# Optimization experiments

Measured on AMD Instinct MI355X. Metric: run time of the kernel, lower is better.

## Reference

```python
import jax, jax.numpy as jnp
import numpy as np

N_HEAD = 16
NEG = -1e9

def setup_inputs() -> dict:
    key = jax.random.key(0)
    ks = jax.random.split(key, 11)
    B, T, D = 2, 2048, 1024
    s = 0.02
    return {
        "x": jax.random.normal(ks[0], (B, T, D), jnp.float32),
        "mask": jax.random.randint(ks[1], (B, T), 0, 2).astype(bool),
        "wq": jax.random.normal(ks[2], (D, D), jnp.float32) * s,
        "bq": jax.random.normal(ks[3], (D,), jnp.float32) * s,
        "wk": jax.random.normal(ks[4], (D, D), jnp.float32) * s,
        "bk": jax.random.normal(ks[5], (D,), jnp.float32) * s,
        "wv": jax.random.normal(ks[6], (D, D), jnp.float32) * s,
        "bv": jax.random.normal(ks[7], (D,), jnp.float32) * s,
        "wp": jax.random.normal(ks[8], (D, D), jnp.float32) * s,
        "bp": jax.random.normal(ks[9], (D,), jnp.float32) * s,
    }

def reference(x, mask, wq, bq, wk, bk, wv, bv, wp, bp):
    B, T, V = x.shape
    H = N_HEAD
    hd = V // H
    # project and split heads: [B, H, T, hd]
    def heads(w, b):
        return (x @ w + b).reshape(B, T, H, hd).transpose(0, 2, 1, 3)
    q = heads(wq, bq)
    k = heads(wk, bk)
    v = heads(wv, bv)
    # scores [B, H, T, T]
    att = jnp.einsum("bhqd,bhkd->bhqk", q, k) * (1.0 / jnp.sqrt(jnp.float32(hd)))
    # key-padding mask: True -> masked. broadcast [B,1,1,T] == torch's [B,1,T,T]
    att = jnp.where(mask[:, None, None, :], NEG, att)
    att = jax.nn.softmax(att, axis=-1)
    out = jnp.einsum("bhqk,bhkd->bhqd", att, v)  # [B,H,T,hd]
    out = out.transpose(0, 2, 1, 3).reshape(B, T, V)
    out = out @ wp + bp
    # dropout is identity in eval mode
    return out, att
```

## Files before the change

### kernel.cpp

```cpp
#include <hip/hip_runtime.h>
#include <stdint.h>
#include <stddef.h>


typedef __attribute__((ext_vector_type(8))) short short8;
typedef __attribute__((ext_vector_type(4))) float f32x4;

#define LDS_AS __attribute__((address_space(3)))
#define GLB_AS __attribute__((address_space(1)))

static __device__ __forceinline__ unsigned short f2bf(float f) {
  union { float f; uint32_t u; } v; v.f = f;
  uint32_t u = v.u;
  return (unsigned short)((u + 0x7fffu + ((u >> 16) & 1u)) >> 16);
}

static __device__ __forceinline__ void gload16(const void* g, void* l) {
  __builtin_amdgcn_global_load_lds((const GLB_AS uint32_t*)g, (LDS_AS uint32_t*)l, 16, 0, 0);
}

static __device__ __forceinline__ f32x4 mfma16(short8 a, short8 b, f32x4 c) {
  return __builtin_amdgcn_mfma_f32_16x16x32_bf16(a, b, c, 0, 0, 0);
}

__global__ void k_convert_x(const float* __restrict__ x, unsigned short* __restrict__ xb) {
  int i = blockIdx.x * 256 + threadIdx.x;
  float4 v = ((const float4*)x)[i];
  ushort4 o;
  o.x = f2bf(v.x); o.y = f2bf(v.y); o.z = f2bf(v.z); o.w = f2bf(v.w);
  ((ushort4*)xb)[i] = o;
}

__global__ void k_mask(const int* __restrict__ m, float* __restrict__ madd) {
  int i = blockIdx.x * 256 + threadIdx.x;
  madd[i] = m[i] ? -1e9f : 0.0f;
}

__global__ void k_transpose_w(const float* __restrict__ w0, const float* __restrict__ w1,
                              const float* __restrict__ w2, const float* __restrict__ w3,
                              unsigned short* __restrict__ o0, unsigned short* __restrict__ o1,
                              unsigned short* __restrict__ o2, unsigned short* __restrict__ o3) {
  int bx = blockIdx.x;
  int which = bx >> 8, tile = bx & 255;
  const float* w = which == 0 ? w0 : which == 1 ? w1 : which == 2 ? w2 : w3;
  unsigned short* o = which == 0 ? o0 : which == 1 ? o1 : which == 2 ? o2 : o3;
  int k0 = (tile >> 4) << 6, n0 = (tile & 15) << 6;
  __shared__ float t[64][65];
  int tid = threadIdx.x;
  int r = tid >> 4, c4 = (tid & 15) << 2;
#pragma unroll
  for (int i = 0; i < 4; i++) {
    int row = r + (i << 4);
    float4 v = *(const float4*)(w + (size_t)(k0 + row) * 1024 + n0 + c4);
    t[row][c4] = v.x; t[row][c4 + 1] = v.y; t[row][c4 + 2] = v.z; t[row][c4 + 3] = v.w;
  }
  __syncthreads();
#pragma unroll
  for (int i = 0; i < 4; i++) {
    int n = r + (i << 4);
    ushort4 ov;
    ov.x = f2bf(t[c4 + 0][n]); ov.y = f2bf(t[c4 + 1][n]);
    ov.z = f2bf(t[c4 + 2][n]); ov.w = f2bf(t[c4 + 3][n]);
    *(ushort4*)(o + (size_t)(n0 + n) * 1024 + k0 + c4) = ov;
  }
}

static __device__ __forceinline__ void gemm_tile(const unsigned short* __restrict__ A,
                                                 const unsigned short* __restrict__ Bt,
                                                 int m0, int n0,
                                                 f32x4 acc[4][4], char* ldsA, char* ldsB) {
  const int tid = threadIdx.x;
  const int l = tid & 63;
  const int wr = tid >> 7;
  const int wc = (tid >> 6) & 1;
  const int arow0 = wr * 64 + (l & 15);
  const int brow0 = wc * 64 + (l & 15);
  const int srow = tid >> 3;
  const int sgi = tid & 7;

  for (int kt = 0; kt < 1024; kt += 64) {
    __syncthreads();
#pragma unroll
    for (int c = 0; c < 4; c++) {
      int row = c * 32 + srow;
      int soff = (sgi ^ (row & 7)) << 3;
      gload16(A + (size_t)(m0 + row) * 1024 + kt + soff, ldsA + (c * 256 + tid) * 16);
      gload16(Bt + (size_t)(n0 + row) * 1024 + kt + soff, ldsB + (c * 256 + tid) * 16);
    }
    asm volatile("s_waitcnt vmcnt(0)" ::: "memory");
    __syncthreads();
#pragma unroll
    for (int ks = 0; ks < 2; ks++) {
      const int kbyte = ks * 64 + ((l >> 4) << 4);
      short8 a[4], b[4];
#pragma unroll
      for (int i = 0; i < 4; i++) {
        int row = arow0 + i * 16;
        a[i] = *(const short8*)(ldsA + row * 128 + (kbyte ^ ((row & 7) << 4)));
      }
#pragma unroll
      for (int j = 0; j < 4; j++) {
        int row = brow0 + j * 16;
        b[j] = *(const short8*)(ldsB + row * 128 + (kbyte ^ ((row & 7) << 4)));
      }
#pragma unroll
      for (int i = 0; i < 4; i++)
#pragma unroll
        for (int j = 0; j < 4; j++)
          acc[i][j] = mfma16(a[i], b[j], acc[i][j]);
    }
  }
}

__global__ __launch_bounds__(256) void k_gemm_qkv(const unsigned short* __restrict__ xb,
    const unsigned short* __restrict__ wqt, const unsigned short* __restrict__ wkt,
    const unsigned short* __restrict__ wvt,
    const float* __restrict__ bq, const float* __restrict__ bk, const float* __restrict__ bv,
    unsigned short* __restrict__ Q, unsigned short* __restrict__ K, unsigned short* __restrict__ Vt) {
  __shared__ __align__(16) char smem[32768];
  char* ldsA = smem;
  char* ldsB = smem + 16384;
  const int mat = blockIdx.y >> 3;
  const int nb = blockIdx.y & 7;
  const unsigned short* Bt = mat == 0 ? wqt : mat == 1 ? wkt : wvt;
  const float* bias = mat == 0 ? bq : mat == 1 ? bk : bv;
  const int m0 = blockIdx.x * 128, n0 = nb * 128;

  f32x4 acc[4][4] = {};
  gemm_tile(xb, Bt, m0, n0, acc, ldsA, ldsB);

  const int tid = threadIdx.x, l = tid & 63;
  const int wr = tid >> 7, wc = (tid >> 6) & 1;
  if (mat < 2) {
    unsigned short* O = (mat == 0) ? Q : K;
#pragma unroll
    for (int j = 0; j < 4; j++) {
      int col = n0 + wc * 64 + j * 16 + (l & 15);
      float bv_ = bias[col];
      int h = col >> 6, d = col & 63;
#pragma unroll
      for (int i = 0; i < 4; i++) {
        int row0 = m0 + wr * 64 + i * 16 + ((l >> 4) << 2);
#pragma unroll
        for (int e = 0; e < 4; e++) {
          int row = row0 + e;
          int b = row >> 11, t = row & 2047;
          O[(((size_t)(b * 16 + h)) * 2048 + t) * 64 + d] = f2bf(acc[i][j][e] + bv_);
        }
      }
    }
  } else {
#pragma unroll
    for (int j = 0; j < 4; j++) {
      int col = n0 + wc * 64 + j * 16 + (l & 15);
      float bv_ = bias[col];
      int h = col >> 6, d = col & 63;
#pragma unroll
      for (int i = 0; i < 4; i++) {
        int row0 = m0 + wr * 64 + i * 16 + ((l >> 4) << 2);
        int b = row0 >> 11, t0 = row0 & 2047;
        ushort4 pk;
        pk.x = f2bf(acc[i][j][0] + bv_);
        pk.y = f2bf(acc[i][j][1] + bv_);
        pk.z = f2bf(acc[i][j][2] + bv_);
        pk.w = f2bf(acc[i][j][3] + bv_);
        *(ushort4*)(Vt + ((size_t)(b * 16 + h) * 64 + d) * 2048 + t0) = pk;
      }
    }
  }
}

__global__ __launch_bounds__(256) void k_gemm_proj(const unsigned short* __restrict__ ctx,
    const unsigned short* __restrict__ wpt, const float* __restrict__ bp,
    float* __restrict__ out) {
  __shared__ __align__(16) char smem[32768];
  char* ldsA = smem;
  char* ldsB = smem + 16384;
  const int m0 = blockIdx.x * 128, n0 = blockIdx.y * 128;
  f32x4 acc[4][4] = {};
  gemm_tile(ctx, wpt, m0, n0, acc, ldsA, ldsB);
  const int tid = threadIdx.x, l = tid & 63;
  const int wr = tid >> 7, wc = (tid >> 6) & 1;
#pragma unroll
  for (int j = 0; j < 4; j++) {
    int col = n0 + wc * 64 + j * 16 + (l & 15);
    float bv_ = bp[col];
#pragma unroll
    for (int i = 0; i < 4; i++) {
      int row0 = m0 + wr * 64 + i * 16 + ((l >> 4) << 2);
#pragma unroll
      for (int e = 0; e < 4; e++)
        out[(size_t)(row0 + e) * 1024 + col] = acc[i][j][e] + bv_;
    }
  }
}

__global__ __launch_bounds__(256) void k_attn(const unsigned short* __restrict__ Q,
    const unsigned short* __restrict__ K, const unsigned short* __restrict__ Vt,
    const float* __restrict__ maskadd, float* __restrict__ att,
    unsigned short* __restrict__ ctx) {
  __shared__ __align__(16) char smem[57344];
  char* Ql = smem;
  char* Kl = smem + 8192;
  char* Vl = smem + 24576;
  char* Pl = smem + 40960;

  const int bid = blockIdx.x;
  const int qb = bid & 31, bh = bid >> 5;
  const int b = bh >> 4, h = bh & 15;
  const int tid = threadIdx.x, w = tid >> 6, l = tid & 63;
  const int qbase = qb * 64;

  const unsigned short* Qg = Q + (size_t)bh * 2048 * 64;
  const unsigned short* Kg = K + (size_t)bh * 2048 * 64;
  const unsigned short* Vg = Vt + (size_t)bh * 64 * 2048;
  const float* mg = maskadd + b * 2048;
  const float scale = 0.125f;

#pragma unroll
  for (int c = 0; c < 2; c++) {
    int g = c * 256 + tid;
    int row = g >> 3, gi = tid & 7;
    gload16(Qg + (size_t)(qbase + row) * 64 + ((gi ^ (row & 7)) << 3), Ql + g * 16);
  }
  asm volatile("s_waitcnt vmcnt(0)" ::: "memory");
  __syncthreads();

  short8 qf[2];
  {
    int row = w * 16 + (l & 15);
#pragma unroll
    for (int ks = 0; ks < 2; ks++) {
      int kbyte = ks * 64 + ((l >> 4) << 4);
      qf[ks] = *(const short8*)(Ql + row * 128 + (kbyte ^ ((row & 7) << 4)));
    }
  }

  float mrow[4], srow[4];
#pragma unroll
  for (int e = 0; e < 4; e++) { mrow[e] = -1e30f; srow[e] = 0.0f; }

  for (int ch = 0; ch < 16; ch++) {
    __syncthreads();
#pragma unroll
    for (int c = 0; c < 4; c++) {
      int g = c * 256 + tid;
      int row = g >> 3, gi = tid & 7;
      gload16(Kg + (size_t)(ch * 128 + row) * 64 + ((gi ^ (row & 7)) << 3), Kl + g * 16);
    }
    asm volatile("s_waitcnt vmcnt(0)" ::: "memory");
    __syncthreads();

    float lv[8][4];
    float cmax[4] = {-1e30f, -1e30f, -1e30f, -1e30f};
#pragma unroll
    for (int nt = 0; nt < 8; nt++) {
      f32x4 s = {};
#pragma unroll
      for (int ks = 0; ks < 2; ks++) {
        int row = nt * 16 + (l & 15);
        int kbyte = ks * 64 + ((l >> 4) << 4);
        short8 kf = *(const short8*)(Kl + row * 128 + (kbyte ^ ((row & 7) << 4)));
        s = mfma16(qf[ks], kf, s);
      }
      int key = ch * 128 + nt * 16 + (l & 15);
      float madd = mg[key];
#pragma unroll
      for (int e = 0; e < 4; e++) {
        lv[nt][e] = s[e] * scale + madd;
        cmax[e] = fmaxf(cmax[e], lv[nt][e]);
      }
    }
#pragma unroll
    for (int e = 0; e < 4; e++) {
      float cs = 0.0f;
#pragma unroll
      for (int nt = 0; nt < 8; nt++) cs += __expf(lv[nt][e] - cmax[e]);
      float mn = fmaxf(mrow[e], cmax[e]);
      srow[e] = srow[e] * __expf(mrow[e] - mn) + cs * __expf(cmax[e] - mn);
      mrow[e] = mn;
    }
  }

  float invs[4];
#pragma unroll
  for (int e = 0; e < 4; e++) {
    float m = mrow[e], s = srow[e];
#pragma unroll
    for (int msk = 1; msk < 16; msk <<= 1) {
      float mo = __shfl_xor(m, msk);
      float so = __shfl_xor(s, msk);
      float mn = fmaxf(m, mo);
      s = s * __expf(m - mn) + so * __expf(mo - mn);
      m = mn;
    }
    mrow[e] = m;
    invs[e] = 1.0f / s;
  }

  f32x4 o[4] = {};
  for (int ch = 0; ch < 16; ch++) {
    __syncthreads();
#pragma unroll
    for (int c = 0; c < 4; c++) {
      int g = c * 256 + tid;
      int row = g >> 3, gi = tid & 7;
      gload16(Kg + (size_t)(ch * 128 + row) * 64 + ((gi ^ (row & 7)) << 3), Kl + g * 16);
    }
#pragma unroll
    for (int c = 0; c < 4; c++) {
      int g = c * 256 + tid;
      int d = g >> 4, gi = tid & 15;
      gload16(Vg + (size_t)d * 2048 + ch * 128 + ((gi ^ (d & 7)) << 3), Vl + g * 16);
    }
    asm volatile("s_waitcnt vmcnt(0)" ::: "memory");
    __syncthreads();

#pragma unroll
    for (int nt = 0; nt < 8; nt++) {
      f32x4 s = {};
#pragma unroll
      for (int ks = 0; ks < 2; ks++) {
        int row = nt * 16 + (l & 15);
        int kbyte = ks * 64 + ((l >> 4) << 4);
        short8 kf = *(const short8*)(Kl + row * 128 + (kbyte ^ ((row & 7) << 4)));
        s = mfma16(qf[ks], kf, s);
      }
      int key = ch * 128 + nt * 16 + (l & 15);
      float madd = mg[key];
#pragma unroll
      for (int e = 0; e < 4; e++) {
        float p = __expf(s[e] * scale + madd - mrow[e]) * invs[e];
        int qrow = qbase + w * 16 + ((l >> 4) << 2) + e;
        att[((size_t)bh * 2048 + qrow) * 2048 + key] = p;
        int pr = w * 16 + ((l >> 4) << 2) + e;
        int cb = (nt * 16 + (l & 15)) * 2;
        *(unsigned short*)(Pl + pr * 256 + (cb ^ ((pr & 7) << 4))) = f2bf(p);
      }
    }
#pragma unroll
    for (int ks = 0; ks < 4; ks++) {
      int prow = w * 16 + (l & 15);
      int kbyte = ks * 64 + ((l >> 4) << 4);
      short8 pa = *(const short8*)(Pl + prow * 256 + (kbyte ^ ((prow & 7) << 4)));
#pragma unroll
      for (int dt = 0; dt < 4; dt++) {
        int vrow = dt * 16 + (l & 15);
        short8 vb = *(const short8*)(Vl + vrow * 256 + (kbyte ^ ((vrow & 7) << 4)));
        o[dt] = mfma16(pa, vb, o[dt]);
      }
    }
  }

#pragma unroll
  for (int dt = 0; dt < 4; dt++) {
#pragma unroll
    for (int e = 0; e < 4; e++) {
      int t = qbase + w * 16 + ((l >> 4) << 2) + e;
      int col = h * 64 + dt * 16 + (l & 15);
      ctx[((size_t)(b * 2048 + t)) * 1024 + col] = f2bf(o[dt][e]);
    }
  }
}

extern "C" void kernel_launch(void* const* d_in, const int* in_sizes, int n_in,
                              void* d_out, int out_size, void* d_ws, size_t ws_size,
                              hipStream_t stream) {
  const float* x  = (const float*)d_in[0];
  const int* mask = (const int*)d_in[1];
  const float* wq = (const float*)d_in[2];
  const float* bq = (const float*)d_in[3];
  const float* wk = (const float*)d_in[4];
  const float* bk = (const float*)d_in[5];
  const float* wv = (const float*)d_in[6];
  const float* bv = (const float*)d_in[7];
  const float* wp = (const float*)d_in[8];
  const float* bp = (const float*)d_in[9];

  float* out = (float*)d_out;
  float* att = out + 4194304;

  char* ws = (char*)d_ws;
  unsigned short* xb  = (unsigned short*)(ws);
  unsigned short* wqt = (unsigned short*)(ws + 8388608);
  unsigned short* wkt = (unsigned short*)(ws + 10485760);
  unsigned short* wvt = (unsigned short*)(ws + 12582912);
  unsigned short* wpt = (unsigned short*)(ws + 14680064);
  unsigned short* Qw  = (unsigned short*)(ws + 16777216);
  unsigned short* Kw  = (unsigned short*)(ws + 25165824);
  unsigned short* Vtw = (unsigned short*)(ws + 33554432);
  unsigned short* ctx = (unsigned short*)(ws + 41943040);
  float* madd         = (float*)(ws + 50331648);

  k_convert_x<<<4096, 256, 0, stream>>>(x, xb);
  k_mask<<<16, 256, 0, stream>>>(mask, madd);
  k_transpose_w<<<1024, 256, 0, stream>>>(wq, wk, wv, wp, wqt, wkt, wvt, wpt);
  k_gemm_qkv<<<dim3(32, 24), 256, 0, stream>>>(xb, wqt, wkt, wvt, bq, bk, bv, Qw, Kw, Vtw);
  k_attn<<<1024, 256, 0, stream>>>(Qw, Kw, Vtw, madd, att, ctx);
  k_gemm_proj<<<dim3(32, 8), 256, 0, stream>>>(ctx, wpt, bp, out);
}
```

Baseline: 276.2 us.

## Stage attention probs in LDS for coalesced stores, double-buffer K, use exp2

Attention probabilities are now written to the fp32 att output from the bf16 P tile in LDS with row-contiguous 16-byte vector stores, instead of scattered per-element stores from the MFMA layout. The P-tile swizzle changes to suit this. The first (statistics) pass double-buffers K tiles across the K and V LDS regions to overlap loads with compute. Scale and mask constants are pre-multiplied by log2(e) so the kernel can use the hardware exp2. Blocks are remapped so consecutive block IDs go to different heads. The risk is that the stored att values are now rounded to bf16 precision, and an extra barrier is added per chunk.

```diff
diff --git a/kernel.cpp b/kernel.cpp
--- a/kernel.cpp
+++ b/kernel.cpp
@@ -13,6 +13,15 @@
   union { float f; uint32_t u; } v; v.f = f;
   uint32_t u = v.u;
   return (unsigned short)((u + 0x7fffu + ((u >> 16) & 1u)) >> 16);
+}
+
+static __device__ __forceinline__ float bf2f(unsigned short h) {
+  union { uint32_t u; float f; } v; v.u = ((uint32_t)h) << 16;
+  return v.f;
+}
+
+static __device__ __forceinline__ float fexp2(float x) {
+  return __builtin_amdgcn_exp2f(x);
 }
 
 static __device__ __forceinline__ void gload16(const void* g, void* l) {
@@ -33,7 +42,7 @@
 
 __global__ void k_mask(const int* __restrict__ m, float* __restrict__ madd) {
   int i = blockIdx.x * 256 + threadIdx.x;
-  madd[i] = m[i] ? -1e9f : 0.0f;
+  madd[i] = m[i] ? -1.44269504e9f : 0.0f;
 }
 
 __global__ void k_transpose_w(const float* __restrict__ w0, const float* __restrict__ w1,
@@ -205,7 +214,7 @@
   char* Vl = smem + 24576;
   char* Pl = smem + 40960;
 
-  const int bid = blockIdx.x;
+  const int bid = (blockIdx.x & 7) * 128 + (blockIdx.x >> 3);
   const int qb = bid & 31, bh = bid >> 5;
   const int b = bh >> 4, h = bh & 15;
   const int tid = threadIdx.x, w = tid >> 6, l = tid & 63;
@@ -215,7 +224,7 @@
   const unsigned short* Kg = K + (size_t)bh * 2048 * 64;
   const unsigned short* Vg = Vt + (size_t)bh * 64 * 2048;
   const float* mg = maskadd + b * 2048;
-  const float scale = 0.125f;
+  const float scale2 = 0.18033688f;
 
 #pragma unroll
   for (int c = 0; c < 2; c++) {
@@ -240,6 +249,81 @@
 #pragma unroll
   for (int e = 0; e < 4; e++) { mrow[e] = -1e30f; srow[e] = 0.0f; }
 
+  {
+#pragma unroll
+    for (int c = 0; c < 4; c++) {
+      int g = c * 256 + tid;
+      int row = g >> 3, gi = tid & 7;
+      gload16(Kg + (size_t)row * 64 + ((gi ^ (row & 7)) << 3), Kl + g * 16);
+    }
+    asm volatile("s_waitcnt vmcnt(0)" ::: "memory");
+    __syncthreads();
+
+    for (int ch = 0; ch < 16; ch++) {
+      char* cur = (ch & 1) ? Vl : Kl;
+      char* nxt = (ch & 1) ? Kl : Vl;
+      if (ch < 15) {
+#pragma unroll
+        for (int c = 0; c < 4; c++) {
+          int g = c * 256 + tid;
+          int row = g >> 3, gi = tid & 7;
+          gload16(Kg + (size_t)((ch + 1) * 128 + row) * 64 + ((gi ^ (row & 7)) << 3),
+                  nxt + g * 16);
+        }
+      }
+
+      float lv[8][4];
+      float cmax[4] = {-1e30f, -1e30f, -1e30f, -1e30f};
+#pragma unroll
+      for (int nt = 0; nt < 8; nt++) {
+        f32x4 s = {};
+#pragma unroll
+        for (int ks = 0; ks < 2; ks++) {
+          int row = nt * 16 + (l & 15);
+          int kbyte = ks * 64 + ((l >> 4) << 4);
+          short8 kf = *(const short8*)(cur + row * 128 + (kbyte ^ ((row & 7) << 4)));
+          s = mfma16(qf[ks], kf, s);
+        }
+        int key = ch * 128 + nt * 16 + (l & 15);
+        float madd = mg[key];
+#pragma unroll
+        for (int e = 0; e < 4; e++) {
+          lv[nt][e] = s[e] * scale2 + madd;
+          cmax[e] = fmaxf(cmax[e], lv[nt][e]);
+        }
+      }
+#pragma unroll
+      for (int e = 0; e < 4; e++) {
+        float cs = 0.0f;
+#pragma unroll
+        for (int nt = 0; nt < 8; nt++) cs += fexp2(lv[nt][e] - cmax[e]);
+        float mn = fmaxf(mrow[e], cmax[e]);
+        srow[e] = srow[e] * fexp2(mrow[e] - mn) + cs * fexp2(cmax[e] - mn);
+        mrow[e] = mn;
+      }
+      asm volatile("s_waitcnt vmcnt(0)" ::: "memory");
+      __syncthreads();
+    }
+  }
+
+  float invs[4];
+#pragma unroll
+  for (int e = 0; e < 4; e++) {
+    float m = mrow[e], s = srow[e];
+#pragma unroll
+    for (int msk = 1; msk < 16; msk <<= 1) {
+      float mo = __shfl_xor(m, msk);
+      float so = __shfl_xor(s, msk);
+      float mn = fmaxf(m, mo);
+      s = s * fexp2(m - mn) + so * fexp2(mo - mn);
+      m = mn;
+    }
+    mrow[e] = m;
+    invs[e] = 1.0f / s;
+  }
+
+  f32x4 o[4] = {};
+  const size_t arowbase = ((size_t)bh * 2048 + qbase) * 2048;
   for (int ch = 0; ch < 16; ch++) {
     __syncthreads();
 #pragma unroll
@@ -248,11 +332,15 @@
       int row = g >> 3, gi = tid & 7;
       gload16(Kg + (size_t)(ch * 128 + row) * 64 + ((gi ^ (row & 7)) << 3), Kl + g * 16);
     }
+#pragma unroll
+    for (int c = 0; c < 4; c++) {
+      int g = c * 256 + tid;
+      int d = g >> 4, gi = tid & 15;
+      gload16(Vg + (size_t)d * 2048 + ch * 128 + ((gi ^ (d & 7)) << 3), Vl + g * 16);
+    }
     asm volatile("s_waitcnt vmcnt(0)" ::: "memory");
     __syncthreads();
 
-    float lv[8][4];
-    float cmax[4] = {-1e30f, -1e30f, -1e30f, -1e30f};
 #pragma unroll
     for (int nt = 0; nt < 8; nt++) {
       f32x4 s = {};
@@ -267,86 +355,39 @@
       float madd = mg[key];
 #pragma unroll
       for (int e = 0; e < 4; e++) {
-        lv[nt][e] = s[e] * scale + madd;
-        cmax[e] = fmaxf(cmax[e], lv[nt][e]);
-      }
-    }
-#pragma unroll
-    for (int e = 0; e < 4; e++) {
-      float cs = 0.0f;
-#pragma unroll
-      for (int nt = 0; nt < 8; nt++) cs += __expf(lv[nt][e] - cmax[e]);
-      float mn = fmaxf(mrow[e], cmax[e]);
-      srow[e] = srow[e] * __expf(mrow[e] - mn) + cs * __expf(cmax[e] - mn);
-      mrow[e] = mn;
-    }
-  }
-
-  float invs[4];
-#pragma unroll
-  for (int e = 0; e < 4; e++) {
-    float m = mrow[e], s = srow[e];
-#pragma unroll
-    for (int msk = 1; msk < 16; msk <<= 1) {
-      float mo = __shfl_xor(m, msk);
-      float so = __shfl_xor(s, msk);
-      float mn = fmaxf(m, mo);
-      s = s * __expf(m - mn) + so * __expf(mo - mn);
-      m = mn;
-    }
-    mrow[e] = m;
-    invs[e] = 1.0f / s;
-  }
-
-  f32x4 o[4] = {};
-  for (int ch = 0; ch < 16; ch++) {
-    __syncthreads();
-#pragma unroll
-    for (int c = 0; c < 4; c++) {
-      int g = c * 256 + tid;
-      int row = g >> 3, gi = tid & 7;
-      gload16(Kg + (size_t)(ch * 128 + row) * 64 + ((gi ^ (row & 7)) << 3), Kl + g * 16);
-    }
-#pragma unroll
-    for (int c = 0; c < 4; c++) {
-      int g = c * 256 + tid;
-      int d = g >> 4, gi = tid & 15;
-      gload16(Vg + (size_t)d * 2048 + ch * 128 + ((gi ^ (d & 7)) << 3), Vl + g * 16);
-    }
-    asm volatile("s_waitcnt vmcnt(0)" ::: "memory");
-    __syncthreads();
-
-#pragma unroll
-    for (int nt = 0; nt < 8; nt++) {
-      f32x4 s = {};
-#pragma unroll
-      for (int ks = 0; ks < 2; ks++) {
-        int row = nt * 16 + (l & 15);
-        int kbyte = ks * 64 + ((l >> 4) << 4);
-        short8 kf = *(const short8*)(Kl + row * 128 + (kbyte ^ ((row & 7) << 4)));
-        s = mfma16(qf[ks], kf, s);
-      }
-      int key = ch * 128 + nt * 16 + (l & 15);
-      float madd = mg[key];
-#pragma unroll
-      for (int e = 0; e < 4; e++) {
-        float p = __expf(s[e] * scale + madd - mrow[e]) * invs[e];
-        int qrow = qbase + w * 16 + ((l >> 4) << 2) + e;
-        att[((size_t)bh * 2048 + qrow) * 2048 + key] = p;
+        float p = fexp2(s[e] * scale2 + madd - mrow[e]) * invs[e];
         int pr = w * 16 + ((l >> 4) << 2) + e;
         int cb = (nt * 16 + (l & 15)) * 2;
-        *(unsigned short*)(Pl + pr * 256 + (cb ^ ((pr & 7) << 4))) = f2bf(p);
-      }
-    }
+        *(unsigned short*)(Pl + pr * 256 + (cb ^ (((pr >> 2) & 3) << 4))) = f2bf(p);
+      }
+    }
+    __syncthreads();
+
+#pragma unroll
+    for (int it = 0; it < 4; it++) {
+      int g = it * 256 + tid;
+      int row = g >> 4, gi = g & 15;
+      short8 pv = *(const short8*)(Pl + row * 256 + ((gi * 16) ^ (((row >> 2) & 3) << 4)));
+      f32x4 lo, hi;
+#pragma unroll
+      for (int j = 0; j < 4; j++) {
+        lo[j] = bf2f((unsigned short)pv[j]);
+        hi[j] = bf2f((unsigned short)pv[4 + j]);
+      }
+      float* dst = att + arowbase + (size_t)row * 2048 + ch * 128 + gi * 8;
+      *(f32x4*)dst = lo;
+      *(f32x4*)(dst + 4) = hi;
+    }
+
 #pragma unroll
     for (int ks = 0; ks < 4; ks++) {
       int prow = w * 16 + (l & 15);
-      int kbyte = ks * 64 + ((l >> 4) << 4);
-      short8 pa = *(const short8*)(Pl + prow * 256 + (kbyte ^ ((prow & 7) << 4)));
+      int kb = ks * 64 + ((l >> 4) << 4);
+      short8 pa = *(const short8*)(Pl + prow * 256 + (kb ^ (((prow >> 2) & 3) << 4)));
 #pragma unroll
       for (int dt = 0; dt < 4; dt++) {
         int vrow = dt * 16 + (l & 15);
-        short8 vb = *(const short8*)(Vl + vrow * 256 + (kbyte ^ ((vrow & 7) << 4)));
+        short8 vb = *(const short8*)(Vl + vrow * 256 + (kb ^ ((vrow & 7) << 4)));
         o[dt] = mfma16(pa, vb, o[dt]);
       }
     }
```

Result: slower. 319.3 us (+15.6%).

## Read Q and K fragments directly from global memory instead of LDS staging

Applied to the files above, without the earlier changes.

Q and K tiles are no longer staged through shared memory. Each lane loads its MFMA fragments straight from global memory, which removes the K load/wait/barrier sequence from the first pass and cuts the LDS footprint from 56KB to 32KB, possibly allowing more blocks per CU. In exchange, each K row is fetched by all four waves separately through the cache rather than once per block, and the loads are no longer overlapped as bulk async copies.

```diff
diff --git a/kernel.cpp b/kernel.cpp
--- a/kernel.cpp
+++ b/kernel.cpp
@@ -199,11 +199,9 @@
     const unsigned short* __restrict__ K, const unsigned short* __restrict__ Vt,
     const float* __restrict__ maskadd, float* __restrict__ att,
     unsigned short* __restrict__ ctx) {
-  __shared__ __align__(16) char smem[57344];
-  char* Ql = smem;
-  char* Kl = smem + 8192;
-  char* Vl = smem + 24576;
-  char* Pl = smem + 40960;
+  __shared__ __align__(16) char smem[32768];
+  char* Vl = smem;
+  char* Pl = smem + 16384;
 
   const int bid = blockIdx.x;
   const int qb = bid & 31, bh = bid >> 5;
@@ -217,23 +215,12 @@
   const float* mg = maskadd + b * 2048;
   const float scale = 0.125f;
 
-#pragma unroll
-  for (int c = 0; c < 2; c++) {
-    int g = c * 256 + tid;
-    int row = g >> 3, gi = tid & 7;
-    gload16(Qg + (size_t)(qbase + row) * 64 + ((gi ^ (row & 7)) << 3), Ql + g * 16);
-  }
-  asm volatile("s_waitcnt vmcnt(0)" ::: "memory");
-  __syncthreads();
-
   short8 qf[2];
   {
-    int row = w * 16 + (l & 15);
-#pragma unroll
-    for (int ks = 0; ks < 2; ks++) {
-      int kbyte = ks * 64 + ((l >> 4) << 4);
-      qf[ks] = *(const short8*)(Ql + row * 128 + (kbyte ^ ((row & 7) << 4)));
-    }
+    int row = qbase + w * 16 + (l & 15);
+#pragma unroll
+    for (int ks = 0; ks < 2; ks++)
+      qf[ks] = *(const short8*)(Qg + (size_t)row * 64 + ks * 32 + ((l >> 4) << 3));
   }
 
   float mrow[4], srow[4];
@@ -241,16 +228,6 @@
   for (int e = 0; e < 4; e++) { mrow[e] = -1e30f; srow[e] = 0.0f; }
 
   for (int ch = 0; ch < 16; ch++) {
-    __syncthreads();
-#pragma unroll
-    for (int c = 0; c < 4; c++) {
-      int g = c * 256 + tid;
-      int row = g >> 3, gi = tid & 7;
-      gload16(Kg + (size_t)(ch * 128 + row) * 64 + ((gi ^ (row & 7)) << 3), Kl + g * 16);
-    }
-    asm volatile("s_waitcnt vmcnt(0)" ::: "memory");
-    __syncthreads();
-
     float lv[8][4];
     float cmax[4] = {-1e30f, -1e30f, -1e30f, -1e30f};
 #pragma unroll
@@ -258,9 +235,8 @@
       f32x4 s = {};
 #pragma unroll
       for (int ks = 0; ks < 2; ks++) {
-        int row = nt * 16 + (l & 15);
-        int kbyte = ks * 64 + ((l >> 4) << 4);
-        short8 kf = *(const short8*)(Kl + row * 128 + (kbyte ^ ((row & 7) << 4)));
+        int row = ch * 128 + nt * 16 + (l & 15);
+        short8 kf = *(const short8*)(Kg + (size_t)row * 64 + ks * 32 + ((l >> 4) << 3));
         s = mfma16(qf[ks], kf, s);
       }
       int key = ch * 128 + nt * 16 + (l & 15);
@@ -304,12 +280,6 @@
 #pragma unroll
     for (int c = 0; c < 4; c++) {
       int g = c * 256 + tid;
-      int row = g >> 3, gi = tid & 7;
-      gload16(Kg + (size_t)(ch * 128 + row) * 64 + ((gi ^ (row & 7)) << 3), Kl + g * 16);
-    }
-#pragma unroll
-    for (int c = 0; c < 4; c++) {
-      int g = c * 256 + tid;
       int d = g >> 4, gi = tid & 15;
       gload16(Vg + (size_t)d * 2048 + ch * 128 + ((gi ^ (d & 7)) << 3), Vl + g * 16);
     }
@@ -321,9 +291,8 @@
       f32x4 s = {};
 #pragma unroll
       for (int ks = 0; ks < 2; ks++) {
-        int row = nt * 16 + (l & 15);
-        int kbyte = ks * 64 + ((l >> 4) << 4);
-        short8 kf = *(const short8*)(Kl + row * 128 + (kbyte ^ ((row & 7) << 4)));
+        int row = ch * 128 + nt * 16 + (l & 15);
+        short8 kf = *(const short8*)(Kg + (size_t)row * 64 + ks * 32 + ((l >> 4) << 3));
         s = mfma16(qf[ks], kf, s);
       }
       int key = ch * 128 + nt * 16 + (l & 15);
@@ -341,12 +310,12 @@
 #pragma unroll
     for (int ks = 0; ks < 4; ks++) {
       int prow = w * 16 + (l & 15);
-      int kbyte = ks * 64 + ((l >> 4) << 4);
-      short8 pa = *(const short8*)(Pl + prow * 256 + (kbyte ^ ((prow & 7) << 4)));
+      int kb = ks * 64 + ((l >> 4) << 4);
+      short8 pa = *(const short8*)(Pl + prow * 256 + (kb ^ ((prow & 7) << 4)));
 #pragma unroll
       for (int dt = 0; dt < 4; dt++) {
         int vrow = dt * 16 + (l & 15);
-        short8 vb = *(const short8*)(Vl + vrow * 256 + (kbyte ^ ((vrow & 7) << 4)));
+        short8 vb = *(const short8*)(Vl + vrow * 256 + (kb ^ ((vrow & 7) << 4)));
         o[dt] = mfma16(pa, vb, o[dt]);
       }
     }
```

Result: slower. 496.3 us (+79.7%).
